# Kernel optimization log

Hardware: AMD Instinct MI355X
Metric: run time of the kernel (lower is better)

## Reference

```python
import jax, jax.numpy as jnp
import numpy as np

N = 50000      # nodes
E = 600000     # edges (avg degree 12)
F_IN = 64      # raw node features
HID = 128      # hidden_size
HEADS = 8
DH = HID // HEADS  # 16, per-head dim = out_channels
C = 10         # classes
L = 3          # num_gnn_layers


def setup_inputs() -> dict:
    key = jax.random.key(0)
    ks = jax.random.split(key, 12)
    g = lambda k, shape, fan: jax.random.normal(k, shape, jnp.float32) / np.float32(np.sqrt(fan))
    return {
        "x": jax.random.normal(ks[0], (N, F_IN), jnp.float32),
        "edge_index": jax.random.randint(ks[1], (2, E), 0, N, dtype=jnp.int32),
        "distance": jax.random.uniform(ks[2], (E, 1), jnp.float32),
        "Wq": g(ks[3], (L, HID, HID), HID), "bq": jnp.zeros((L, HID), jnp.float32),
        "Wk": g(ks[4], (L, HID, HID), HID), "bk": jnp.zeros((L, HID), jnp.float32),
        "Wv": g(ks[5], (L, HID, HID), HID), "bv": jnp.zeros((L, HID), jnp.float32),
        "We": g(ks[6], (L, 1, HID), 1),
        "Ws": g(ks[7], (L, HID, HID), HID), "bs": jnp.zeros((L, HID), jnp.float32),
        "ln_g": jnp.ones((L, HID), jnp.float32), "ln_b": jnp.zeros((L, HID), jnp.float32),
        "W_before": g(ks[8], (F_IN, HID), F_IN), "b_before": jnp.zeros((HID,), jnp.float32),
        "W_after": g(ks[9], (HID, C), HID), "b_after": jnp.zeros((C,), jnp.float32),
    }


def _layer_norm(h, gamma, beta):
    m = h.mean(-1, keepdims=True)
    v = ((h - m) ** 2).mean(-1, keepdims=True)
    return (h - m) * jax.lax.rsqrt(v + 1e-5) * gamma + beta


def _transformer_conv(h, src, dst, ea, Wq, bq, Wk, bk, Wv, bv, We, Ws, bs):
    # PyG TransformerConv (concat=True, beta=False, root_weight=True), eval mode (no dropout)
    q = (h @ Wq + bq).reshape(-1, HEADS, DH)   # [N,H,D]
    k = (h @ Wk + bk).reshape(-1, HEADS, DH)
    v = (h @ Wv + bv).reshape(-1, HEADS, DH)
    e = (ea @ We).reshape(-1, HEADS, DH)       # [E,H,D] edge embedding (no bias)
    ke = k[src] + e                            # gather keys along edges
    alpha = (q[dst] * ke).sum(-1) / np.float32(np.sqrt(DH))  # [E,H]
    # segment softmax over incoming edges per destination node
    amax = jax.ops.segment_max(alpha, dst, num_segments=N)
    amax = jnp.where(jnp.isfinite(amax), amax, 0.0)
    ex = jnp.exp(alpha - amax[dst])
    den = jax.ops.segment_sum(ex, dst, num_segments=N)
    a = ex / (den[dst] + 1e-16)                # [E,H]
    msg = (v[src] + e) * a[..., None]          # weighted values
    out = jax.ops.segment_sum(msg, dst, num_segments=N).reshape(-1, HEADS * DH)
    return out + h @ Ws + bs                   # root/skip connection


def reference(x, edge_index, distance, Wq, bq, Wk, bk, Wv, bv, We, Ws, bs,
              ln_g, ln_b, W_before, b_before, W_after, b_after):
    src, dst = edge_index[0], edge_index[1]
    h = jax.nn.relu(x @ W_before + b_before)   # fcnn_before
    for i in range(L):
        h = _transformer_conv(h, src, dst, distance,
                              Wq[i], bq[i], Wk[i], bk[i], Wv[i], bv[i],
                              We[i], Ws[i], bs[i])
        if i < L - 1:
            h = jax.nn.relu(_layer_norm(h, ln_g[i], ln_b[i]))
    # fcnn_after
    h = jax.nn.relu(_layer_norm(h, ln_g[L - 1], ln_b[L - 1]))
    h = h @ W_after + b_after
    return jax.nn.log_softmax(h, axis=1)
```

## Files before the change

### kernel.cpp

```cpp
#include <hip/hip_runtime.h>
#include <cstdint>
#include <cstddef>

#define NN 50000
#define NE 600000
#define FIN 64
#define HID 128
#define NCLS 10
#define NLAYER 3

#define QSCALE 0.36067376022224085f

typedef __bf16 bf16x8 __attribute__((ext_vector_type(8)));
typedef float f32x4 __attribute__((ext_vector_type(4)));
typedef float f32x2 __attribute__((ext_vector_type(2)));

__device__ __forceinline__ unsigned short f2bf(float f) {
    unsigned int u = __builtin_bit_cast(unsigned int, f);
    u += 0x7fffu + ((u >> 16) & 1u);
    return (unsigned short)(u >> 16);
}
__device__ __forceinline__ float bf2f(unsigned short s) {
    unsigned int u = ((unsigned int)s) << 16;
    return __builtin_bit_cast(float, u);
}
__device__ __forceinline__ float lo16f(unsigned int w) {
    return __builtin_bit_cast(float, w << 16);
}
__device__ __forceinline__ float hi16f(unsigned int w) {
    return __builtin_bit_cast(float, w & 0xffff0000u);
}

__global__ __launch_bounds__(256) void k_count(const int* __restrict__ edst,
                                               int* __restrict__ counts) {
    int e = blockIdx.x * 256 + threadIdx.x;
    if (e < NE) atomicAdd(&counts[edst[e]], 1);
}

__global__ __launch_bounds__(512) void k_scan1(const int* __restrict__ counts,
                                               int* __restrict__ row_ptr,
                                               int* __restrict__ partials, int n) {
    __shared__ int sm[512];
    int tid = threadIdx.x;
    int i = blockIdx.x * 512 + tid;
    int v = (i < n) ? counts[i] : 0;
    sm[tid] = v;
    __syncthreads();
    #pragma unroll
    for (int off = 1; off < 512; off <<= 1) {
        int t = (tid >= off) ? sm[tid - off] : 0;
        __syncthreads();
        sm[tid] += t;
        __syncthreads();
    }
    if (i < n) row_ptr[i] = sm[tid] - v;
    if (tid == 511) partials[blockIdx.x] = sm[511];
}

__global__ __launch_bounds__(128) void k_scan2(int* __restrict__ partials, int nb) {
    __shared__ int sm[128];
    int t = threadIdx.x;
    int v = (t < nb) ? partials[t] : 0;
    sm[t] = v;
    __syncthreads();
    #pragma unroll
    for (int off = 1; off < 128; off <<= 1) {
        int x = (t >= off) ? sm[t - off] : 0;
        __syncthreads();
        sm[t] += x;
        __syncthreads();
    }
    if (t < nb) partials[t] = sm[t] - v;
}

__global__ __launch_bounds__(512) void k_scan3(int* __restrict__ row_ptr,
                                               const int* __restrict__ partials, int n) {
    int i = blockIdx.x * 512 + threadIdx.x;
    if (i < n) row_ptr[i] += partials[blockIdx.x];
}

__global__ __launch_bounds__(256) void k_fill(const int* __restrict__ esrc,
                                              const int* __restrict__ edst,
                                              const float* __restrict__ dist,
                                              int* __restrict__ cursor,
                                              const int* __restrict__ row_ptr,
                                              int2* __restrict__ srcd) {
    int e = blockIdx.x * 256 + threadIdx.x;
    if (e < NE) {
        int d = edst[e];
        int pos = atomicAdd(&cursor[d], 1);
        srcd[row_ptr[d] + pos] = make_int2(esrc[e], __float_as_int(dist[e]));
    }
}

__global__ __launch_bounds__(256) void k_wprep(
    const float* __restrict__ Wq, const float* __restrict__ Wk,
    const float* __restrict__ Wv, const float* __restrict__ Ws,
    const float* __restrict__ Wbe, const float* __restrict__ Waf,
    unsigned short* __restrict__ Wt12,
    unsigned short* __restrict__ Wbt,
    float* __restrict__ Wat)
{
    int blk = blockIdx.x;
    int tid = threadIdx.x;
    if (blk < 768) {
        int m = blk >> 6;
        int l = m >> 2, which = m & 3;
        const float* src;
        if (which == 0) src = Wq; else if (which == 1) src = Wk;
        else if (which == 2) src = Wv; else src = Ws;
        src += (size_t)l * HID * HID;
        int idx = (blk & 63) * 256 + tid;
        int c = idx >> 7, k = idx & 127;
        Wt12[(size_t)m * 16384 + (size_t)c * 128 + k] = f2bf(src[(size_t)k * 128 + c]);
    } else if (blk < 800) {
        int idx = (blk - 768) * 256 + tid;
        int c = idx >> 6, k = idx & 63;
        Wbt[(size_t)c * 64 + k] = f2bf(Wbe[(size_t)k * 128 + c]);
    } else {
        int i = (blk - 800) * 256 + tid;
        if (i < 1280) {
            int c = i >> 7, f = i & 127;
            Wat[i] = Waf[f * 10 + c];
        }
    }
}

__global__ __launch_bounds__(512) void k_qkvs(
    const unsigned short* __restrict__ Ab, int nrows,
    const unsigned short* __restrict__ Wt,
    const float* __restrict__ bq, const float* __restrict__ bk,
    const float* __restrict__ bv, const float* __restrict__ bs,
    unsigned short* __restrict__ qb,
    unsigned char* __restrict__ kv8,
    unsigned short* __restrict__ hsb)
{
    const int tid = threadIdx.x;
    const int w = tid >> 6, lane = tid & 63;
    const int m = w >> 1, ch = w & 1;
    const float* bias = (m == 0) ? bq : (m == 1) ? bk : (m == 2) ? bv : bs;
    const unsigned short* Wm = Wt + (size_t)m * 16384;
    const int lc = lane & 15, lk = lane >> 4;

    bf16x8 b[4][4];
    float bb[4];
    #pragma unroll
    for (int ct = 0; ct < 4; ++ct) {
        int col = ch * 64 + ct * 16 + lc;
        bb[ct] = bias[col];
        #pragma unroll
        for (int kb = 0; kb < 4; ++kb)
            b[ct][kb] = *(const bf16x8*)(Wm + (size_t)col * 128 + kb * 32 + lk * 8);
    }

    const int r0 = blockIdx.x * 64;
    #pragma unroll
    for (int rt = 0; rt < 4; ++rt) {
        const int arow = r0 + rt * 16 + lc;
        bf16x8 z = {};
        bf16x8 a[4];
        #pragma unroll
        for (int kb = 0; kb < 4; ++kb)
            a[kb] = (arow < nrows) ? *(const bf16x8*)(Ab + (size_t)arow * 128 + kb * 32 + lk * 8) : z;
        #pragma unroll
        for (int ct = 0; ct < 4; ++ct) {
            f32x4 acc = {0.f, 0.f, 0.f, 0.f};
            #pragma unroll
            for (int kb = 0; kb < 4; ++kb)
                acc = __builtin_amdgcn_mfma_f32_16x16x32_bf16(a[kb], b[ct][kb], acc, 0, 0, 0);
            const int col = ch * 64 + ct * 16 + lc;
            #pragma unroll
            for (int i = 0; i < 4; ++i) {
                int r = r0 + rt * 16 + lk * 4 + i;
                if (r >= nrows) continue;
                float val = acc[i] + bb[ct];
                if (m == 0) {
                    qb[(size_t)r * 128 + col] = f2bf(val * QSCALE);
                } else if (m == 1) {
                    unsigned int pk = __builtin_amdgcn_cvt_pk_fp8_f32(val, val, 0, false);
                    kv8[(size_t)r * 256 + col] = (unsigned char)(pk & 0xff);
                } else if (m == 2) {
                    unsigned int pk = __builtin_amdgcn_cvt_pk_fp8_f32(val, val, 0, false);
                    kv8[(size_t)r * 256 + 128 + col] = (unsigned char)(pk & 0xff);
                } else {
                    hsb[(size_t)r * 128 + col] = f2bf(val);
                }
            }
        }
    }
}

__global__ __launch_bounds__(256) void k_gin(
    const float* __restrict__ x, int nrows,
    const unsigned short* __restrict__ Wt,
    const float* __restrict__ bias,
    unsigned short* __restrict__ hb)
{
    const int tid = threadIdx.x;
    const int w = tid >> 6, lane = tid & 63;
    const int row0 = blockIdx.x * 64 + w * 16;
    const int lc = lane & 15, lk = lane >> 4;
    const int arow = row0 + lc;
    const bool rv = arow < nrows;

    bf16x8 a[2];
    #pragma unroll
    for (int kb = 0; kb < 2; ++kb) {
        union { bf16x8 v; unsigned short u[8]; } t;
        #pragma unroll
        for (int q = 0; q < 2; ++q) {
            float4 f = rv ? *(const float4*)(x + (size_t)arow * 64 + kb * 32 + lk * 8 + q * 4)
                          : make_float4(0.f, 0.f, 0.f, 0.f);
            t.u[q * 4 + 0] = f2bf(f.x); t.u[q * 4 + 1] = f2bf(f.y);
            t.u[q * 4 + 2] = f2bf(f.z); t.u[q * 4 + 3] = f2bf(f.w);
        }
        a[kb] = t.v;
    }

    const int cbase = lk * 4;
    #pragma unroll
    for (int ct = 0; ct < 8; ++ct) {
        const int bcol = ct * 16 + lc;
        f32x4 acc = {0.f, 0.f, 0.f, 0.f};
        #pragma unroll
        for (int kb = 0; kb < 2; ++kb) {
            bf16x8 b = *(const bf16x8*)(Wt + (size_t)bcol * 64 + kb * 32 + lk * 8);
            acc = __builtin_amdgcn_mfma_f32_16x16x32_bf16(a[kb], b, acc, 0, 0, 0);
        }
        const float bv_ = bias[bcol];
        #pragma unroll
        for (int i = 0; i < 4; ++i) {
            int r = row0 + cbase + i;
            if (r >= nrows) continue;
            hb[(size_t)r * 128 + bcol] = f2bf(fmaxf(acc[i] + bv_, 0.f));
        }
    }
}

#define LOADB(bi, kw, vw, dd, vv) {                                       \
    int rel_ = (bi) * 8 + j;                                              \
    vv = rel_ < cnt;                                                      \
    if (vv) {                                                             \
        int2 e2_ = srcd[beg + rel_];                                      \
        dd = __int_as_float(e2_.y);                                       \
        const unsigned char* kr_ = kvb + (size_t)e2_.x * 256 + h * 16;    \
        *(uint4*)(kw) = *(const uint4*)(kr_);                             \
        *(uint4*)(vw) = *(const uint4*)(kr_ + 128);                       \
    } else {                                                              \
        dd = 0.f;                                                         \
        _Pragma("unroll")                                                 \
        for (int z_ = 0; z_ < 4; ++z_) { (kw)[z_] = 0u; (vw)[z_] = 0u; }  \
    } }

#define COMPB(kw, vw, dd, vv) {                                           \
    float p_ = 0.f;                                                       \
    _Pragma("unroll")                                                     \
    for (int w4 = 0; w4 < 4; ++w4) {                                      \
        f32x2 k01_ = __builtin_amdgcn_cvt_pk_f32_fp8((kw)[w4], false);    \
        f32x2 k23_ = __builtin_amdgcn_cvt_pk_f32_fp8((kw)[w4], true);     \
        p_ = fmaf(qf[4 * w4 + 0], k01_.x, p_);                            \
        p_ = fmaf(qf[4 * w4 + 1], k01_.y, p_);                            \
        p_ = fmaf(qf[4 * w4 + 2], k23_.x, p_);                            \
        p_ = fmaf(qf[4 * w4 + 3], k23_.y, p_);                            \
    }                                                                     \
    p_ = fmaf(dd, qwe, p_);                                               \
    float wgt_ = (vv) ? exp2f(p_) : 0.f;                                  \
    s += wgt_;                                                            \
    sd = fmaf(dd, wgt_, sd);                                              \
    _Pragma("unroll")                                                     \
    for (int w4 = 0; w4 < 4; ++w4) {                                      \
        f32x2 v01_ = __builtin_amdgcn_cvt_pk_f32_fp8((vw)[w4], false);    \
        f32x2 v23_ = __builtin_amdgcn_cvt_pk_f32_fp8((vw)[w4], true);     \
        vacc[4 * w4 + 0] = fmaf(v01_.x, wgt_, vacc[4 * w4 + 0]);          \
        vacc[4 * w4 + 1] = fmaf(v01_.y, wgt_, vacc[4 * w4 + 1]);          \
        vacc[4 * w4 + 2] = fmaf(v23_.x, wgt_, vacc[4 * w4 + 2]);          \
        vacc[4 * w4 + 3] = fmaf(v23_.y, wgt_, vacc[4 * w4 + 3]);          \
    } }

template <int LAST>
__global__ __launch_bounds__(256) void k_attn(
    const unsigned short* __restrict__ qb,
    const unsigned short* __restrict__ hsb,
    const unsigned char* __restrict__ kvb,
    const int2* __restrict__ srcd,
    const float* __restrict__ We,
    const int* __restrict__ row_ptr,
    const float* __restrict__ lng,
    const float* __restrict__ lnb,
    unsigned short* __restrict__ hb,
    const float* __restrict__ Wat,
    const float* __restrict__ ba,
    float* __restrict__ out, int nnodes)
{
    const int wid = threadIdx.x >> 6;
    const int lane = threadIdx.x & 63;
    const int n = blockIdx.x * 4 + wid;
    if (n >= nnodes) return;
    const int h = lane >> 3, j = lane & 7;
    const int c0 = lane * 2;

    unsigned int uq[8];
    *(uint4*)(uq)     = *(const uint4*)(qb + (size_t)n * 128 + h * 16);
    *(uint4*)(uq + 4) = *(const uint4*)(qb + (size_t)n * 128 + h * 16 + 8);
    float qf[16];
    #pragma unroll
    for (int d = 0; d < 8; ++d) {
        qf[2 * d]     = lo16f(uq[d]);
        qf[2 * d + 1] = hi16f(uq[d]);
    }
    float qwe = 0.f;
    #pragma unroll
    for (int d4 = 0; d4 < 4; ++d4) {
        float4 wv = *(const float4*)(We + h * 16 + d4 * 4);
        qwe = fmaf(qf[d4 * 4 + 0], wv.x, qwe);
        qwe = fmaf(qf[d4 * 4 + 1], wv.y, qwe);
        qwe = fmaf(qf[d4 * 4 + 2], wv.z, qwe);
        qwe = fmaf(qf[d4 * 4 + 3], wv.w, qwe);
    }

    const int beg = row_ptr[n];
    const int cnt = row_ptr[n + 1] - beg;
    float s = 0.f, sd = 0.f;
    float vacc[16];
    #pragma unroll
    for (int d = 0; d < 16; ++d) vacc[d] = 0.f;

    if (cnt > 0) {
        const int nbatch = (cnt + 7) >> 3;
        unsigned int kwA[4], vwA[4], kwB[4], vwB[4], kwC[4], vwC[4];
        float dA = 0.f, dB = 0.f, dC = 0.f;
        bool vA = false, vB = false, vC = false;
        LOADB(0, kwA, vwA, dA, vA);
        if (1 < nbatch) LOADB(1, kwB, vwB, dB, vB);
        int b = 0;
        while (true) {
            if (b + 2 < nbatch) LOADB(b + 2, kwC, vwC, dC, vC);
            COMPB(kwA, vwA, dA, vA);
            if (++b >= nbatch) break;
            if (b + 2 < nbatch) LOADB(b + 2, kwA, vwA, dA, vA);
            COMPB(kwB, vwB, dB, vB);
            if (++b >= nbatch) break;
            if (b + 2 < nbatch) LOADB(b + 2, kwB, vwB, dB, vB);
            COMPB(kwC, vwC, dC, vC);
            if (++b >= nbatch) break;
        }
    }

    #pragma unroll
    for (int msk = 1; msk < 8; msk <<= 1) {
        s  += __shfl_xor(s, msk);
        sd += __shfl_xor(sd, msk);
    }
    const bool b4 = (lane & 4) != 0;
    float c8[8];
    #pragma unroll
    for (int i = 0; i < 8; ++i) {
        float sendv = b4 ? vacc[i] : vacc[8 + i];
        float keep  = b4 ? vacc[8 + i] : vacc[i];
        c8[i] = keep + __shfl_xor(sendv, 4);
    }
    const bool b2 = (lane & 2) != 0;
    float c4[4];
    #pragma unroll
    for (int i = 0; i < 4; ++i) {
        float sendv = b2 ? c8[i] : c8[4 + i];
        float keep  = b2 ? c8[4 + i] : c8[i];
        c4[i] = keep + __shfl_xor(sendv, 2);
    }
    const bool b1 = (lane & 1) != 0;
    float c2[2];
    #pragma unroll
    for (int i = 0; i < 2; ++i) {
        float sendv = b1 ? c4[i] : c4[2 + i];
        float keep  = b1 ? c4[2 + i] : c4[i];
        c2[i] = keep + __shfl_xor(sendv, 1);
    }

    const float inv = 1.f / (s + 1e-16f);
    const float we0 = We[c0], we1 = We[c0 + 1];
    const ushort2 hu = *(const ushort2*)(hsb + (size_t)n * 128 + c0);
    float o0 = fmaf(fmaf(we0, sd, c2[0]), inv, bf2f(hu.x));
    float o1 = fmaf(fmaf(we1, sd, c2[1]), inv, bf2f(hu.y));

    float t = o0 + o1;
    #pragma unroll
    for (int off = 1; off < 64; off <<= 1) t += __shfl_xor(t, off);
    float mean = t * 0.0078125f;
    float d0 = o0 - mean, d1 = o1 - mean;
    float vv2 = d0 * d0 + d1 * d1;
    #pragma unroll
    for (int off = 1; off < 64; off <<= 1) vv2 += __shfl_xor(vv2, off);
    float rstd = rsqrtf(vv2 * 0.0078125f + 1e-5f);
    float y0 = fmaxf(d0 * rstd * lng[c0] + lnb[c0], 0.f);
    float y1 = fmaxf(d1 * rstd * lng[c0 + 1] + lnb[c0 + 1], 0.f);

    if (LAST) {
        float lg[NCLS];
        #pragma unroll
        for (int c = 0; c < NCLS; ++c) {
            float2 wv = *(const float2*)(Wat + c * 128 + c0);
            float p = fmaf(y0, wv.x, y1 * wv.y);
            #pragma unroll
            for (int msk = 1; msk < 64; msk <<= 1) p += __shfl_xor(p, msk);
            lg[c] = p + ba[c];
        }
        float mx = lg[0];
        #pragma unroll
        for (int c = 1; c < NCLS; ++c) mx = fmaxf(mx, lg[c]);
        float sum = 0.f;
        #pragma unroll
        for (int c = 0; c < NCLS; ++c) sum += __expf(lg[c] - mx);
        float lse = mx + __logf(sum);
        if (lane == 0) {
            #pragma unroll
            for (int c = 0; c < NCLS; ++c) out[(size_t)n * NCLS + c] = lg[c] - lse;
        }
    } else {
        ushort2 o;
        o.x = f2bf(y0);
        o.y = f2bf(y1);
        *(ushort2*)(hb + (size_t)n * 128 + c0) = o;
    }
}

extern "C" void kernel_launch(void* const* d_in, const int* in_sizes, int n_in,
                              void* d_out, int out_size, void* d_ws, size_t ws_size,
                              hipStream_t stream)
{
    const float* x    = (const float*)d_in[0];
    const int*   ei   = (const int*)d_in[1];
    const float* dist = (const float*)d_in[2];
    const float* Wq   = (const float*)d_in[3];
    const float* bq   = (const float*)d_in[4];
    const float* Wk   = (const float*)d_in[5];
    const float* bk   = (const float*)d_in[6];
    const float* Wv   = (const float*)d_in[7];
    const float* bv   = (const float*)d_in[8];
    const float* We   = (const float*)d_in[9];
    const float* Wsk  = (const float*)d_in[10];
    const float* bs   = (const float*)d_in[11];
    const float* lng  = (const float*)d_in[12];
    const float* lnb  = (const float*)d_in[13];
    const float* Wbe  = (const float*)d_in[14];
    const float* bbe  = (const float*)d_in[15];
    const float* Waf  = (const float*)d_in[16];
    const float* baf  = (const float*)d_in[17];
    float* out = (float*)d_out;
    const int* esrc = ei;
    const int* edst = ei + NE;

    char* ws = (char*)d_ws;
    size_t off = 0;
    unsigned short* qb  = (unsigned short*)(ws + off); off += 12800000;
    unsigned short* hsb = (unsigned short*)(ws + off); off += 12800000;
    unsigned char*  kv8 = (unsigned char*)(ws + off);  off += 12800000;
    unsigned short* hb  = (unsigned short*)(ws + off); off += 12800000;
    unsigned short* Wt12 = (unsigned short*)(ws + off); off += 393216;
    unsigned short* Wbt  = (unsigned short*)(ws + off); off += 16384;
    float* Wat = (float*)(ws + off);   off += 5120;
    int* counts   = (int*)(ws + off);  off += 200192;
    int* cursor   = (int*)(ws + off);  off += 200192;
    int* row_ptr  = (int*)(ws + off);  off += 200192;
    int* partials = (int*)(ws + off);  off += 512;
    int2* srcd    = (int2*)(ws + off); off += (size_t)NE * 8;

    hipMemsetAsync(counts, 0, (NN + 1) * sizeof(int), stream);
    hipMemsetAsync(cursor, 0, NN * sizeof(int), stream);
    k_count<<<(NE + 255) / 256, 256, 0, stream>>>(edst, counts);
    int nsb = (NN + 1 + 511) / 512;
    k_scan1<<<nsb, 512, 0, stream>>>(counts, row_ptr, partials, NN + 1);
    k_scan2<<<1, 128, 0, stream>>>(partials, nsb);
    k_scan3<<<nsb, 512, 0, stream>>>(row_ptr, partials, NN + 1);
    k_fill<<<(NE + 255) / 256, 256, 0, stream>>>(esrc, edst, dist, cursor, row_ptr, srcd);

    k_wprep<<<805, 256, 0, stream>>>(Wq, Wk, Wv, Wsk, Wbe, Waf, Wt12, Wbt, Wat);

    const int ngb = (NN + 63) / 64;

    k_gin<<<ngb, 256, 0, stream>>>(x, NN, Wbt, bbe, hb);

    for (int l = 0; l < NLAYER; ++l) {
        const unsigned short* wt = Wt12 + (size_t)l * 4 * 16384;
        k_qkvs<<<ngb, 512, 0, stream>>>(hb, NN, wt,
            bq + l * HID, bk + l * HID, bv + l * HID, bs + l * HID,
            qb, kv8, hsb);
        if (l < NLAYER - 1) {
            k_attn<0><<<(NN + 3) / 4, 256, 0, stream>>>(qb, hsb, kv8, srcd, We + l * HID,
                row_ptr, lng + l * HID, lnb + l * HID, hb, nullptr, nullptr, nullptr, NN);
        } else {
            k_attn<1><<<(NN + 3) / 4, 256, 0, stream>>>(qb, hsb, kv8, srcd, We + l * HID,
                row_ptr, lng + l * HID, lnb + l * HID, hb, Wat, baf, out, NN);
        }
    }
}
```

Before: 396.1 us.

## Interleave fp8 K/V per 4-col chunk and split attention lanes by edge halves

Attention now gives each lane four feature columns across all heads, with the two half-waves processing alternate edges. This replaces the old one-head-per-8-lanes batching and its butterfly shuffle reduction. K and V are stored interleaved in 4-byte chunks so one 8-byte load per lane fetches both. The QKV and input GEMMs swap MFMA operands so each lane writes four contiguous outputs as vector stores. The edge-count kernel is merged into the weight-prep kernel and the two memsets are combined, cutting launches, at the cost of an extra shuffle per edge for the head dot product.

```diff
diff --git a/kernel.cpp b/kernel.cpp
--- a/kernel.cpp
+++ b/kernel.cpp
@@ -24,82 +24,15 @@
     unsigned int u = ((unsigned int)s) << 16;
     return __builtin_bit_cast(float, u);
 }
-__device__ __forceinline__ float lo16f(unsigned int w) {
-    return __builtin_bit_cast(float, w << 16);
-}
-__device__ __forceinline__ float hi16f(unsigned int w) {
-    return __builtin_bit_cast(float, w & 0xffff0000u);
-}
-
-__global__ __launch_bounds__(256) void k_count(const int* __restrict__ edst,
-                                               int* __restrict__ counts) {
-    int e = blockIdx.x * 256 + threadIdx.x;
-    if (e < NE) atomicAdd(&counts[edst[e]], 1);
-}
-
-__global__ __launch_bounds__(512) void k_scan1(const int* __restrict__ counts,
-                                               int* __restrict__ row_ptr,
-                                               int* __restrict__ partials, int n) {
-    __shared__ int sm[512];
-    int tid = threadIdx.x;
-    int i = blockIdx.x * 512 + tid;
-    int v = (i < n) ? counts[i] : 0;
-    sm[tid] = v;
-    __syncthreads();
-    #pragma unroll
-    for (int off = 1; off < 512; off <<= 1) {
-        int t = (tid >= off) ? sm[tid - off] : 0;
-        __syncthreads();
-        sm[tid] += t;
-        __syncthreads();
-    }
-    if (i < n) row_ptr[i] = sm[tid] - v;
-    if (tid == 511) partials[blockIdx.x] = sm[511];
-}
-
-__global__ __launch_bounds__(128) void k_scan2(int* __restrict__ partials, int nb) {
-    __shared__ int sm[128];
-    int t = threadIdx.x;
-    int v = (t < nb) ? partials[t] : 0;
-    sm[t] = v;
-    __syncthreads();
-    #pragma unroll
-    for (int off = 1; off < 128; off <<= 1) {
-        int x = (t >= off) ? sm[t - off] : 0;
-        __syncthreads();
-        sm[t] += x;
-        __syncthreads();
-    }
-    if (t < nb) partials[t] = sm[t] - v;
-}
-
-__global__ __launch_bounds__(512) void k_scan3(int* __restrict__ row_ptr,
-                                               const int* __restrict__ partials, int n) {
-    int i = blockIdx.x * 512 + threadIdx.x;
-    if (i < n) row_ptr[i] += partials[blockIdx.x];
-}
-
-__global__ __launch_bounds__(256) void k_fill(const int* __restrict__ esrc,
-                                              const int* __restrict__ edst,
-                                              const float* __restrict__ dist,
-                                              int* __restrict__ cursor,
-                                              const int* __restrict__ row_ptr,
-                                              int2* __restrict__ srcd) {
-    int e = blockIdx.x * 256 + threadIdx.x;
-    if (e < NE) {
-        int d = edst[e];
-        int pos = atomicAdd(&cursor[d], 1);
-        srcd[row_ptr[d] + pos] = make_int2(esrc[e], __float_as_int(dist[e]));
-    }
-}
-
-__global__ __launch_bounds__(256) void k_wprep(
+
+__global__ __launch_bounds__(256) void k_prep(
     const float* __restrict__ Wq, const float* __restrict__ Wk,
     const float* __restrict__ Wv, const float* __restrict__ Ws,
     const float* __restrict__ Wbe, const float* __restrict__ Waf,
     unsigned short* __restrict__ Wt12,
     unsigned short* __restrict__ Wbt,
-    float* __restrict__ Wat)
+    float* __restrict__ Wat,
+    const int* __restrict__ edst, int* __restrict__ counts)
 {
     int blk = blockIdx.x;
     int tid = threadIdx.x;
@@ -117,12 +50,71 @@
         int idx = (blk - 768) * 256 + tid;
         int c = idx >> 6, k = idx & 63;
         Wbt[(size_t)c * 64 + k] = f2bf(Wbe[(size_t)k * 128 + c]);
-    } else {
+    } else if (blk < 805) {
         int i = (blk - 800) * 256 + tid;
         if (i < 1280) {
             int c = i >> 7, f = i & 127;
             Wat[i] = Waf[f * 10 + c];
         }
+    } else {
+        int e = (blk - 805) * 256 + tid;
+        if (e < NE) atomicAdd(&counts[edst[e]], 1);
+    }
+}
+
+__global__ __launch_bounds__(512) void k_scan1(const int* __restrict__ counts,
+                                               int* __restrict__ row_ptr,
+                                               int* __restrict__ partials, int n) {
+    __shared__ int sm[512];
+    int tid = threadIdx.x;
+    int i = blockIdx.x * 512 + tid;
+    int v = (i < n) ? counts[i] : 0;
+    sm[tid] = v;
+    __syncthreads();
+    #pragma unroll
+    for (int off = 1; off < 512; off <<= 1) {
+        int t = (tid >= off) ? sm[tid - off] : 0;
+        __syncthreads();
+        sm[tid] += t;
+        __syncthreads();
+    }
+    if (i < n) row_ptr[i] = sm[tid] - v;
+    if (tid == 511) partials[blockIdx.x] = sm[511];
+}
+
+__global__ __launch_bounds__(128) void k_scan2(int* __restrict__ partials, int nb) {
+    __shared__ int sm[128];
+    int t = threadIdx.x;
+    int v = (t < nb) ? partials[t] : 0;
+    sm[t] = v;
+    __syncthreads();
+    #pragma unroll
+    for (int off = 1; off < 128; off <<= 1) {
+        int x = (t >= off) ? sm[t - off] : 0;
+        __syncthreads();
+        sm[t] += x;
+        __syncthreads();
+    }
+    if (t < nb) partials[t] = sm[t] - v;
+}
+
+__global__ __launch_bounds__(512) void k_scan3(int* __restrict__ row_ptr,
+                                               const int* __restrict__ partials, int n) {
+    int i = blockIdx.x * 512 + threadIdx.x;
+    if (i < n) row_ptr[i] += partials[blockIdx.x];
+}
+
+__global__ __launch_bounds__(256) void k_fill(const int* __restrict__ esrc,
+                                              const int* __restrict__ edst,
+                                              const float* __restrict__ dist,
+                                              int* __restrict__ cursor,
+                                              const int* __restrict__ row_ptr,
+                                              int2* __restrict__ srcd) {
+    int e = blockIdx.x * 256 + threadIdx.x;
+    if (e < NE) {
+        int d = edst[e];
+        int pos = atomicAdd(&cursor[d], 1);
+        srcd[row_ptr[d] + pos] = make_int2(esrc[e], __float_as_int(dist[e]));
     }
 }
 
@@ -142,48 +134,50 @@
     const unsigned short* Wm = Wt + (size_t)m * 16384;
     const int lc = lane & 15, lk = lane >> 4;
 
-    bf16x8 b[4][4];
-    float bb[4];
+    bf16x8 bw[4][4];
+    float4 bb[4];
     #pragma unroll
     for (int ct = 0; ct < 4; ++ct) {
         int col = ch * 64 + ct * 16 + lc;
-        bb[ct] = bias[col];
+        bb[ct] = *(const float4*)(bias + ch * 64 + ct * 16 + lk * 4);
         #pragma unroll
         for (int kb = 0; kb < 4; ++kb)
-            b[ct][kb] = *(const bf16x8*)(Wm + (size_t)col * 128 + kb * 32 + lk * 8);
+            bw[ct][kb] = *(const bf16x8*)(Wm + (size_t)col * 128 + kb * 32 + lk * 8);
     }
 
     const int r0 = blockIdx.x * 64;
     #pragma unroll
     for (int rt = 0; rt < 4; ++rt) {
         const int arow = r0 + rt * 16 + lc;
+        const bool rv = arow < nrows;
         bf16x8 z = {};
         bf16x8 a[4];
         #pragma unroll
         for (int kb = 0; kb < 4; ++kb)
-            a[kb] = (arow < nrows) ? *(const bf16x8*)(Ab + (size_t)arow * 128 + kb * 32 + lk * 8) : z;
+            a[kb] = rv ? *(const bf16x8*)(Ab + (size_t)arow * 128 + kb * 32 + lk * 8) : z;
         #pragma unroll
         for (int ct = 0; ct < 4; ++ct) {
             f32x4 acc = {0.f, 0.f, 0.f, 0.f};
             #pragma unroll
             for (int kb = 0; kb < 4; ++kb)
-                acc = __builtin_amdgcn_mfma_f32_16x16x32_bf16(a[kb], b[ct][kb], acc, 0, 0, 0);
-            const int col = ch * 64 + ct * 16 + lc;
-            #pragma unroll
-            for (int i = 0; i < 4; ++i) {
-                int r = r0 + rt * 16 + lk * 4 + i;
-                if (r >= nrows) continue;
-                float val = acc[i] + bb[ct];
+                acc = __builtin_amdgcn_mfma_f32_16x16x32_bf16(bw[ct][kb], a[kb], acc, 0, 0, 0);
+            if (rv) {
+                const int colb = ch * 64 + ct * 16 + lk * 4;
+                float v0 = acc[0] + bb[ct].x, v1 = acc[1] + bb[ct].y;
+                float v2 = acc[2] + bb[ct].z, v3 = acc[3] + bb[ct].w;
                 if (m == 0) {
-                    qb[(size_t)r * 128 + col] = f2bf(val * QSCALE);
-                } else if (m == 1) {
-                    unsigned int pk = __builtin_amdgcn_cvt_pk_fp8_f32(val, val, 0, false);
-                    kv8[(size_t)r * 256 + col] = (unsigned char)(pk & 0xff);
-                } else if (m == 2) {
-                    unsigned int pk = __builtin_amdgcn_cvt_pk_fp8_f32(val, val, 0, false);
-                    kv8[(size_t)r * 256 + 128 + col] = (unsigned char)(pk & 0xff);
+                    ushort4 o;
+                    o.x = f2bf(v0 * QSCALE); o.y = f2bf(v1 * QSCALE);
+                    o.z = f2bf(v2 * QSCALE); o.w = f2bf(v3 * QSCALE);
+                    *(ushort4*)(qb + (size_t)arow * 128 + colb) = o;
+                } else if (m == 1 || m == 2) {
+                    unsigned int pk = __builtin_amdgcn_cvt_pk_fp8_f32(v0, v1, 0, false);
+                    pk = __builtin_amdgcn_cvt_pk_fp8_f32(v2, v3, pk, true);
+                    *(unsigned int*)(kv8 + (size_t)arow * 256 + (colb >> 2) * 8 + (m == 2 ? 4 : 0)) = pk;
                 } else {
-                    hsb[(size_t)r * 128 + col] = f2bf(val);
+                    ushort4 o;
+                    o.x = f2bf(v0); o.y = f2bf(v1); o.z = f2bf(v2); o.w = f2bf(v3);
+                    *(ushort4*)(hsb + (size_t)arow * 128 + colb) = o;
                 }
             }
         }
@@ -198,9 +192,8 @@
 {
     const int tid = threadIdx.x;
     const int w = tid >> 6, lane = tid & 63;
-    const int row0 = blockIdx.x * 64 + w * 16;
     const int lc = lane & 15, lk = lane >> 4;
-    const int arow = row0 + lc;
+    const int arow = blockIdx.x * 64 + w * 16 + lc;
     const bool rv = arow < nrows;
 
     bf16x8 a[2];
@@ -217,71 +210,53 @@
         a[kb] = t.v;
     }
 
-    const int cbase = lk * 4;
     #pragma unroll
     for (int ct = 0; ct < 8; ++ct) {
-        const int bcol = ct * 16 + lc;
         f32x4 acc = {0.f, 0.f, 0.f, 0.f};
         #pragma unroll
         for (int kb = 0; kb < 2; ++kb) {
-            bf16x8 b = *(const bf16x8*)(Wt + (size_t)bcol * 64 + kb * 32 + lk * 8);
-            acc = __builtin_amdgcn_mfma_f32_16x16x32_bf16(a[kb], b, acc, 0, 0, 0);
-        }
-        const float bv_ = bias[bcol];
-        #pragma unroll
-        for (int i = 0; i < 4; ++i) {
-            int r = row0 + cbase + i;
-            if (r >= nrows) continue;
-            hb[(size_t)r * 128 + bcol] = f2bf(fmaxf(acc[i] + bv_, 0.f));
-        }
-    }
-}
-
-#define LOADB(bi, kw, vw, dd, vv) {                                       \
-    int rel_ = (bi) * 8 + j;                                              \
-    vv = rel_ < cnt;                                                      \
-    if (vv) {                                                             \
-        int2 e2_ = srcd[beg + rel_];                                      \
-        dd = __int_as_float(e2_.y);                                       \
-        const unsigned char* kr_ = kvb + (size_t)e2_.x * 256 + h * 16;    \
-        *(uint4*)(kw) = *(const uint4*)(kr_);                             \
-        *(uint4*)(vw) = *(const uint4*)(kr_ + 128);                       \
-    } else {                                                              \
-        dd = 0.f;                                                         \
-        _Pragma("unroll")                                                 \
-        for (int z_ = 0; z_ < 4; ++z_) { (kw)[z_] = 0u; (vw)[z_] = 0u; }  \
-    } }
-
-#define COMPB(kw, vw, dd, vv) {                                           \
-    float p_ = 0.f;                                                       \
-    _Pragma("unroll")                                                     \
-    for (int w4 = 0; w4 < 4; ++w4) {                                      \
-        f32x2 k01_ = __builtin_amdgcn_cvt_pk_f32_fp8((kw)[w4], false);    \
-        f32x2 k23_ = __builtin_amdgcn_cvt_pk_f32_fp8((kw)[w4], true);     \
-        p_ = fmaf(qf[4 * w4 + 0], k01_.x, p_);                            \
-        p_ = fmaf(qf[4 * w4 + 1], k01_.y, p_);                            \
-        p_ = fmaf(qf[4 * w4 + 2], k23_.x, p_);                            \
-        p_ = fmaf(qf[4 * w4 + 3], k23_.y, p_);                            \
-    }                                                                     \
-    p_ = fmaf(dd, qwe, p_);                                               \
-    float wgt_ = (vv) ? exp2f(p_) : 0.f;                                  \
-    s += wgt_;                                                            \
-    sd = fmaf(dd, wgt_, sd);                                              \
-    _Pragma("unroll")                                                     \
-    for (int w4 = 0; w4 < 4; ++w4) {                                      \
-        f32x2 v01_ = __builtin_amdgcn_cvt_pk_f32_fp8((vw)[w4], false);    \
-        f32x2 v23_ = __builtin_amdgcn_cvt_pk_f32_fp8((vw)[w4], true);     \
-        vacc[4 * w4 + 0] = fmaf(v01_.x, wgt_, vacc[4 * w4 + 0]);          \
-        vacc[4 * w4 + 1] = fmaf(v01_.y, wgt_, vacc[4 * w4 + 1]);          \
-        vacc[4 * w4 + 2] = fmaf(v23_.x, wgt_, vacc[4 * w4 + 2]);          \
-        vacc[4 * w4 + 3] = fmaf(v23_.y, wgt_, vacc[4 * w4 + 3]);          \
-    } }
+            bf16x8 bwf = *(const bf16x8*)(Wt + (size_t)(ct * 16 + lc) * 64 + kb * 32 + lk * 8);
+            acc = __builtin_amdgcn_mfma_f32_16x16x32_bf16(bwf, a[kb], acc, 0, 0, 0);
+        }
+        if (rv) {
+            float4 bv_ = *(const float4*)(bias + ct * 16 + lk * 4);
+            ushort4 o;
+            o.x = f2bf(fmaxf(acc[0] + bv_.x, 0.f));
+            o.y = f2bf(fmaxf(acc[1] + bv_.y, 0.f));
+            o.z = f2bf(fmaxf(acc[2] + bv_.z, 0.f));
+            o.w = f2bf(fmaxf(acc[3] + bv_.w, 0.f));
+            *(ushort4*)(hb + (size_t)arow * 128 + ct * 16 + lk * 4) = o;
+        }
+    }
+}
+
+#define FETCHE(t, sreg, kreg, ereg) {                                     \
+    int rel_ = 2 * (t) + half;                                            \
+    ereg = rel_ < cnt;                                                    \
+    sreg = srcd[beg + (ereg ? rel_ : 0)];                                 \
+    kreg = *(const uint2*)(kv8 + (size_t)sreg.x * 256 + l5 * 8); }
+
+#define COMPE(sreg, kreg, ereg) {                                         \
+    float dd_ = __int_as_float(sreg.y);                                   \
+    f32x2 k01_ = __builtin_amdgcn_cvt_pk_f32_fp8(kreg.x, false);          \
+    f32x2 k23_ = __builtin_amdgcn_cvt_pk_f32_fp8(kreg.x, true);           \
+    float p_ = q0 * k01_.x + q1 * k01_.y + q2 * k23_.x + q3 * k23_.y;     \
+    p_ += __shfl_xor(p_, 1);                                              \
+    p_ += __shfl_xor(p_, 2);                                              \
+    p_ = fmaf(dd_, qwe, p_);                                              \
+    float w_ = (ereg) ? exp2f(p_) : 0.f;                                  \
+    s += w_;                                                              \
+    sd = fmaf(dd_, w_, sd);                                               \
+    f32x2 v01_ = __builtin_amdgcn_cvt_pk_f32_fp8(kreg.y, false);          \
+    f32x2 v23_ = __builtin_amdgcn_cvt_pk_f32_fp8(kreg.y, true);           \
+    va0 = fmaf(v01_.x, w_, va0); va1 = fmaf(v01_.y, w_, va1);             \
+    va2 = fmaf(v23_.x, w_, va2); va3 = fmaf(v23_.y, w_, va3); }
 
 template <int LAST>
-__global__ __launch_bounds__(256) void k_attn(
+__global__ __launch_bounds__(256, 6) void k_attn(
     const unsigned short* __restrict__ qb,
     const unsigned short* __restrict__ hsb,
-    const unsigned char* __restrict__ kvb,
+    const unsigned char* __restrict__ kv8,
     const int2* __restrict__ srcd,
     const float* __restrict__ We,
     const int* __restrict__ row_ptr,
@@ -296,112 +271,82 @@
     const int lane = threadIdx.x & 63;
     const int n = blockIdx.x * 4 + wid;
     if (n >= nnodes) return;
-    const int h = lane >> 3, j = lane & 7;
-    const int c0 = lane * 2;
-
-    unsigned int uq[8];
-    *(uint4*)(uq)     = *(const uint4*)(qb + (size_t)n * 128 + h * 16);
-    *(uint4*)(uq + 4) = *(const uint4*)(qb + (size_t)n * 128 + h * 16 + 8);
-    float qf[16];
-    #pragma unroll
-    for (int d = 0; d < 8; ++d) {
-        qf[2 * d]     = lo16f(uq[d]);
-        qf[2 * d + 1] = hi16f(uq[d]);
-    }
-    float qwe = 0.f;
-    #pragma unroll
-    for (int d4 = 0; d4 < 4; ++d4) {
-        float4 wv = *(const float4*)(We + h * 16 + d4 * 4);
-        qwe = fmaf(qf[d4 * 4 + 0], wv.x, qwe);
-        qwe = fmaf(qf[d4 * 4 + 1], wv.y, qwe);
-        qwe = fmaf(qf[d4 * 4 + 2], wv.z, qwe);
-        qwe = fmaf(qf[d4 * 4 + 3], wv.w, qwe);
-    }
+    const int half = lane >> 5;
+    const int l5 = lane & 31;
+    const int d0 = l5 * 4;
 
     const int beg = row_ptr[n];
     const int cnt = row_ptr[n + 1] - beg;
+
+    ushort4 qu = *(const ushort4*)(qb + (size_t)n * 128 + d0);
+    const float q0 = bf2f(qu.x), q1 = bf2f(qu.y), q2 = bf2f(qu.z), q3 = bf2f(qu.w);
+    const float4 wv = *(const float4*)(We + d0);
+    float qwe = q0 * wv.x + q1 * wv.y + q2 * wv.z + q3 * wv.w;
+    qwe += __shfl_xor(qwe, 1);
+    qwe += __shfl_xor(qwe, 2);
+
     float s = 0.f, sd = 0.f;
-    float vacc[16];
-    #pragma unroll
-    for (int d = 0; d < 16; ++d) vacc[d] = 0.f;
+    float va0 = 0.f, va1 = 0.f, va2 = 0.f, va3 = 0.f;
 
     if (cnt > 0) {
-        const int nbatch = (cnt + 7) >> 3;
-        unsigned int kwA[4], vwA[4], kwB[4], vwB[4], kwC[4], vwC[4];
-        float dA = 0.f, dB = 0.f, dC = 0.f;
-        bool vA = false, vB = false, vC = false;
-        LOADB(0, kwA, vwA, dA, vA);
-        if (1 < nbatch) LOADB(1, kwB, vwB, dB, vB);
-        int b = 0;
+        const int niter = (cnt + 1) >> 1;
+        int2 sA, sB, sC;
+        uint2 kA, kB, kC;
+        bool eA, eB, eC;
+        FETCHE(0, sA, kA, eA);
+        if (1 < niter) FETCHE(1, sB, kB, eB);
+        int t = 0;
         while (true) {
-            if (b + 2 < nbatch) LOADB(b + 2, kwC, vwC, dC, vC);
-            COMPB(kwA, vwA, dA, vA);
-            if (++b >= nbatch) break;
-            if (b + 2 < nbatch) LOADB(b + 2, kwA, vwA, dA, vA);
-            COMPB(kwB, vwB, dB, vB);
-            if (++b >= nbatch) break;
-            if (b + 2 < nbatch) LOADB(b + 2, kwB, vwB, dB, vB);
-            COMPB(kwC, vwC, dC, vC);
-            if (++b >= nbatch) break;
-        }
-    }
-
-    #pragma unroll
-    for (int msk = 1; msk < 8; msk <<= 1) {
-        s  += __shfl_xor(s, msk);
-        sd += __shfl_xor(sd, msk);
-    }
-    const bool b4 = (lane & 4) != 0;
-    float c8[8];
-    #pragma unroll
-    for (int i = 0; i < 8; ++i) {
-        float sendv = b4 ? vacc[i] : vacc[8 + i];
-        float keep  = b4 ? vacc[8 + i] : vacc[i];
-        c8[i] = keep + __shfl_xor(sendv, 4);
-    }
-    const bool b2 = (lane & 2) != 0;
-    float c4[4];
-    #pragma unroll
-    for (int i = 0; i < 4; ++i) {
-        float sendv = b2 ? c8[i] : c8[4 + i];
-        float keep  = b2 ? c8[4 + i] : c8[i];
-        c4[i] = keep + __shfl_xor(sendv, 2);
-    }
-    const bool b1 = (lane & 1) != 0;
-    float c2[2];
-    #pragma unroll
-    for (int i = 0; i < 2; ++i) {
-        float sendv = b1 ? c4[i] : c4[2 + i];
-        float keep  = b1 ? c4[2 + i] : c4[i];
-        c2[i] = keep + __shfl_xor(sendv, 1);
-    }
+            if (t + 2 < niter) FETCHE(t + 2, sC, kC, eC);
+            COMPE(sA, kA, eA);
+            if (++t >= niter) break;
+            if (t + 2 < niter) FETCHE(t + 2, sA, kA, eA);
+            COMPE(sB, kB, eB);
+            if (++t >= niter) break;
+            if (t + 2 < niter) FETCHE(t + 2, sB, kB, eB);
+            COMPE(sC, kC, eC);
+            if (++t >= niter) break;
+        }
+    }
+
+    s  += __shfl_xor(s, 32);
+    sd += __shfl_xor(sd, 32);
+    va0 += __shfl_xor(va0, 32);
+    va1 += __shfl_xor(va1, 32);
+    va2 += __shfl_xor(va2, 32);
+    va3 += __shfl_xor(va3, 32);
 
     const float inv = 1.f / (s + 1e-16f);
-    const float we0 = We[c0], we1 = We[c0 + 1];
-    const ushort2 hu = *(const ushort2*)(hsb + (size_t)n * 128 + c0);
-    float o0 = fmaf(fmaf(we0, sd, c2[0]), inv, bf2f(hu.x));
-    float o1 = fmaf(fmaf(we1, sd, c2[1]), inv, bf2f(hu.y));
-
-    float t = o0 + o1;
-    #pragma unroll
-    for (int off = 1; off < 64; off <<= 1) t += __shfl_xor(t, off);
-    float mean = t * 0.0078125f;
-    float d0 = o0 - mean, d1 = o1 - mean;
-    float vv2 = d0 * d0 + d1 * d1;
-    #pragma unroll
-    for (int off = 1; off < 64; off <<= 1) vv2 += __shfl_xor(vv2, off);
-    float rstd = rsqrtf(vv2 * 0.0078125f + 1e-5f);
-    float y0 = fmaxf(d0 * rstd * lng[c0] + lnb[c0], 0.f);
-    float y1 = fmaxf(d1 * rstd * lng[c0 + 1] + lnb[c0 + 1], 0.f);
+    const ushort4 hu = *(const ushort4*)(hsb + (size_t)n * 128 + d0);
+    float o0 = fmaf(fmaf(wv.x, sd, va0), inv, bf2f(hu.x));
+    float o1 = fmaf(fmaf(wv.y, sd, va1), inv, bf2f(hu.y));
+    float o2 = fmaf(fmaf(wv.z, sd, va2), inv, bf2f(hu.z));
+    float o3 = fmaf(fmaf(wv.w, sd, va3), inv, bf2f(hu.w));
+
+    float tt = o0 + o1 + o2 + o3;
+    #pragma unroll
+    for (int msk = 1; msk < 32; msk <<= 1) tt += __shfl_xor(tt, msk);
+    const float mean = tt * 0.0078125f;
+    const float e0 = o0 - mean, e1 = o1 - mean, e2 = o2 - mean, e3 = o3 - mean;
+    float vv2 = e0 * e0 + e1 * e1 + e2 * e2 + e3 * e3;
+    #pragma unroll
+    for (int msk = 1; msk < 32; msk <<= 1) vv2 += __shfl_xor(vv2, msk);
+    const float rstd = rsqrtf(vv2 * 0.0078125f + 1e-5f);
+    const float4 g4 = *(const float4*)(lng + d0);
+    const float4 b4 = *(const float4*)(lnb + d0);
+    const float y0 = fmaxf(fmaf(e0 * rstd, g4.x, b4.x), 0.f);
+    const float y1 = fmaxf(fmaf(e1 * rstd, g4.y, b4.y), 0.f);
+    const float y2 = fmaxf(fmaf(e2 * rstd, g4.z, b4.z), 0.f);
+    const float y3 = fmaxf(fmaf(e3 * rstd, g4.w, b4.w), 0.f);
 
     if (LAST) {
         float lg[NCLS];
         #pragma unroll
         for (int c = 0; c < NCLS; ++c) {
-            float2 wv = *(const float2*)(Wat + c * 128 + c0);
-            float p = fmaf(y0, wv.x, y1 * wv.y);
+            float4 wa = *(const float4*)(Wat + c * 128 + d0);
+            float p = y0 * wa.x + y1 * wa.y + y2 * wa.z + y3 * wa.w;
             #pragma unroll
-            for (int msk = 1; msk < 64; msk <<= 1) p += __shfl_xor(p, msk);
+            for (int msk = 1; msk < 32; msk <<= 1) p += __shfl_xor(p, msk);
             lg[c] = p + ba[c];
         }
         float mx = lg[0];
@@ -415,11 +360,10 @@
             #pragma unroll
             for (int c = 0; c < NCLS; ++c) out[(size_t)n * NCLS + c] = lg[c] - lse;
         }
-    } else {
-        ushort2 o;
-        o.x = f2bf(y0);
-        o.y = f2bf(y1);
-        *(ushort2*)(hb + (size_t)n * 128 + c0) = o;
+    } else if (lane < 32) {
+        ushort4 o;
+        o.x = f2bf(y0); o.y = f2bf(y1); o.z = f2bf(y2); o.w = f2bf(y3);
+        *(ushort4*)(hb + (size_t)n * 128 + d0) = o;
     }
 }
 
@@ -464,17 +408,15 @@
     int* partials = (int*)(ws + off);  off += 512;
     int2* srcd    = (int2*)(ws + off); off += (size_t)NE * 8;
 
-    hipMemsetAsync(counts, 0, (NN + 1) * sizeof(int), stream);
-    hipMemsetAsync(cursor, 0, NN * sizeof(int), stream);
-    k_count<<<(NE + 255) / 256, 256, 0, stream>>>(edst, counts);
+    hipMemsetAsync(counts, 0, 2 * 200192, stream);
+    k_prep<<<805 + (NE + 255) / 256, 256, 0, stream>>>(
+        Wq, Wk, Wv, Wsk, Wbe, Waf, Wt12, Wbt, Wat, edst, counts);
     int nsb = (NN + 1 + 511) / 512;
     k_scan1<<<nsb, 512, 0, stream>>>(counts, row_ptr, partials, NN + 1);
     k_scan2<<<1, 128, 0, stream>>>(partials, nsb);
     k_scan3<<<nsb, 512, 0, stream>>>(row_ptr, partials, NN + 1);
     k_fill<<<(NE + 255) / 256, 256, 0, stream>>>(esrc, edst, dist, cursor, row_ptr, srcd);
 
-    k_wprep<<<805, 256, 0, stream>>>(Wq, Wk, Wv, Wsk, Wbe, Waf, Wt12, Wbt, Wat);
-
     const int ngb = (NN + 63) / 64;
 
     k_gin<<<ngb, 256, 0, stream>>>(x, NN, Wbt, bbe, hb);
@@ -484,11 +426,12 @@
         k_qkvs<<<ngb, 512, 0, stream>>>(hb, NN, wt,
             bq + l * HID, bk + l * HID, bv + l * HID, bs + l * HID,
             qb, kv8, hsb);
+        const int nab = (NN + 3) / 4;
         if (l < NLAYER - 1) {
-            k_attn<0><<<(NN + 3) / 4, 256, 0, stream>>>(qb, hsb, kv8, srcd, We + l * HID,
+            k_attn<0><<<nab, 256, 0, stream>>>(qb, hsb, kv8, srcd, We + l * HID,
                 row_ptr, lng + l * HID, lnb + l * HID, hb, nullptr, nullptr, nullptr, NN);
         } else {
-            k_attn<1><<<(NN + 3) / 4, 256, 0, stream>>>(qb, hsb, kv8, srcd, We + l * HID,
+            k_attn<1><<<nab, 256, 0, stream>>>(qb, hsb, kv8, srcd, We + l * HID,
                 row_ptr, lng + l * HID, lnb + l * HID, hb, Wat, baf, out, NN);
         }
     }
```

Measured after the change: 358.9 us. -9.4%, faster.
